# Optimization experiments

Hardware: AMD Instinct MI355X
Metric: run time of the kernel (lower is better)

The kernel has to match this reference:

```python
import jax, jax.numpy as jnp
import numpy as np

D_MODEL = 1024
D_STATE = 16
EXPAND = 2
D_CONV = 4
D_INNER = EXPAND * D_MODEL          # 2048
DT_RANK = D_MODEL // 16             # 64
B = 2
L = 1024
EPS = 1e-5


def setup_inputs() -> dict:
    key = jax.random.key(0)
    ks = jax.random.split(key, 8)
    s = 0.02
    return {
        "x": jax.random.normal(ks[0], (B, L, D_MODEL), jnp.float32),
        "ln_gamma": jnp.ones((D_MODEL,), jnp.float32),
        "ln_beta": jnp.zeros((D_MODEL,), jnp.float32),
        "in_proj_w": jax.random.normal(ks[1], (2 * D_INNER, D_MODEL), jnp.float32) * s,
        "conv_w": jax.random.normal(ks[2], (D_INNER, 1, D_CONV), jnp.float32) * s,
        "conv_b": jnp.zeros((D_INNER,), jnp.float32),
        "x_proj_w": jax.random.normal(ks[3], (DT_RANK + 2 * D_STATE, D_INNER), jnp.float32) * s,
        "dt_proj_w": jax.random.normal(ks[4], (D_INNER, DT_RANK), jnp.float32) * s,
        "dt_proj_b": jax.random.normal(ks[5], (D_INNER,), jnp.float32) * 0.01,
        "A_log": jnp.log(jnp.tile(jnp.arange(1, D_STATE + 1, dtype=jnp.float32), (D_INNER, 1))),
        "D_skip": jnp.ones((D_INNER,), jnp.float32),
        "out_proj_w": jax.random.normal(ks[6], (D_MODEL, D_INNER), jnp.float32) * s,
    }


def _layernorm(x, g, b):
    mu = jnp.mean(x, axis=-1, keepdims=True)
    var = jnp.mean((x - mu) ** 2, axis=-1, keepdims=True)
    return (x - mu) * jax.lax.rsqrt(var + EPS) * g + b


def _mamba_forward(x, ln_gamma, ln_beta, in_proj_w, conv_w, conv_b,
                   x_proj_w, dt_proj_w, dt_proj_b, A_log, D_skip, out_proj_w):
    residual = x
    xn = _layernorm(x, ln_gamma, ln_beta)

    # in_proj -> split into ssm input u and gate z   (b, l, 2*d_inner)
    xz = jnp.einsum('bld,ed->ble', xn, in_proj_w)
    u, z = jnp.split(xz, 2, axis=-1)

    # causal depthwise conv1d (padding = d_conv-1 on the left, truncated to L)
    uc = jnp.transpose(u, (0, 2, 1))  # (b, d_inner, l)
    uc = jax.lax.conv_general_dilated(
        uc, conv_w, window_strides=(1,), padding=[(D_CONV - 1, 0)],
        feature_group_count=D_INNER,
        dimension_numbers=('NCH', 'OIH', 'NCH'))
    uc = uc + conv_b[None, :, None]
    u = jax.nn.silu(jnp.transpose(uc, (0, 2, 1)))  # (b, l, d_inner)

    # selective SSM
    A = -jnp.exp(A_log)                              # (d_inner, d_state)
    x_dbl = jnp.einsum('bld,ed->ble', u, x_proj_w)   # (b, l, dt_rank+2*n)
    dt, Bm, Cm = jnp.split(x_dbl, [DT_RANK, DT_RANK + D_STATE], axis=-1)
    delta = jax.nn.softplus(jnp.einsum('blr,dr->bld', dt, dt_proj_w) + dt_proj_b)

    def step(h, inputs):
        d_t, B_t, C_t, u_t = inputs            # (b,di) (b,n) (b,n) (b,di)
        dA = jnp.exp(d_t[..., None] * A)       # (b, di, n)
        h = dA * h + (d_t * u_t)[..., None] * B_t[:, None, :]
        y = jnp.einsum('bdn,bn->bd', h, C_t)
        return h, y

    h0 = jnp.zeros((x.shape[0], D_INNER, D_STATE), x.dtype)
    xs = (jnp.moveaxis(delta, 1, 0), jnp.moveaxis(Bm, 1, 0),
          jnp.moveaxis(Cm, 1, 0), jnp.moveaxis(u, 1, 0))
    _, ys = jax.lax.scan(step, h0, xs)
    y = jnp.moveaxis(ys, 0, 1) + u * D_skip     # (b, l, d_inner)

    y = y * jax.nn.silu(z)                      # gated output
    out = jnp.einsum('ble,de->bld', y, out_proj_w)
    # dropout is identity in eval mode
    return out + residual


def reference(x, ln_gamma, ln_beta, in_proj_w, conv_w, conv_b,
              x_proj_w, dt_proj_w, dt_proj_b, A_log, D_skip, out_proj_w):
    return _mamba_forward(x, ln_gamma, ln_beta, in_proj_w, conv_w, conv_b,
                          x_proj_w, dt_proj_w, dt_proj_b, A_log, D_skip, out_proj_w)
```

## Files before the change

### kernel.cpp

```cpp
#include <hip/hip_runtime.h>

#define D_MODEL 1024
#define D_STATE 16
#define D_INNER 2048
#define DT_RANK 64
#define NBATCH 2
#define SEQ_L 1024
#define M_ROWS (NBATCH * SEQ_L)
#define CHUNK 32
#define NCHUNK (SEQ_L / CHUNK)

typedef __bf16 bf16x8 __attribute__((ext_vector_type(8)));
typedef float f32x4 __attribute__((ext_vector_type(4)));
typedef unsigned short u16;
typedef unsigned int u32;
typedef u16 u16x4 __attribute__((ext_vector_type(4)));
typedef u16 u16x8 __attribute__((ext_vector_type(8)));

__device__ __forceinline__ float bf2f(u16 h) {
    return __uint_as_float(((unsigned)h) << 16);
}
__device__ __forceinline__ u16 f2bf(float f) {
    unsigned u = __float_as_uint(f);
    u += 0x7fff + ((u >> 16) & 1);
    return (u16)(u >> 16);
}

__global__ __launch_bounds__(256) void prep(
    const float* __restrict__ s0, const float* __restrict__ s1,
    const float* __restrict__ s2, const float* __restrict__ s3,
    u16* __restrict__ d0, u16* __restrict__ d1,
    u16* __restrict__ d2, u16* __restrict__ d3,
    const float* __restrict__ x, const float* __restrict__ g,
    const float* __restrict__ b, u16* __restrict__ xn) {
    int blk = blockIdx.x;
    if (blk < 6464) {
        int idx = blk * 256 + threadIdx.x;
        const float4* s; u16* dp; int i;
        if (idx < 1048576)      { s = (const float4*)s0; i = idx;           dp = d0; }
        else if (idx < 1572864) { s = (const float4*)s1; i = idx - 1048576; dp = d1; }
        else if (idx < 1622016) { s = (const float4*)s2; i = idx - 1572864; dp = d2; }
        else                    { s = (const float4*)s3; i = idx - 1622016; dp = d3; }
        float4 v = s[i];
        u16x4 o = {f2bf(v.x), f2bf(v.y), f2bf(v.z), f2bf(v.w)};
        *(u16x4*)(dp + (size_t)i * 4) = o;
        return;
    }
    int row = blk - 6464;
    const float4* xr = (const float4*)(x + (size_t)row * D_MODEL);
    float4 v = xr[threadIdx.x];
    float s  = v.x + v.y + v.z + v.w;
    float ss = v.x * v.x + v.y * v.y + v.z * v.z + v.w * v.w;
#pragma unroll
    for (int off = 32; off > 0; off >>= 1) {
        s  += __shfl_down(s,  off, 64);
        ss += __shfl_down(ss, off, 64);
    }
    __shared__ float sh_s[4], sh_ss[4];
    int wid = threadIdx.x >> 6;
    if ((threadIdx.x & 63) == 0) { sh_s[wid] = s; sh_ss[wid] = ss; }
    __syncthreads();
    float mu  = (sh_s[0] + sh_s[1] + sh_s[2] + sh_s[3]) * (1.0f / D_MODEL);
    float var = (sh_ss[0] + sh_ss[1] + sh_ss[2] + sh_ss[3]) * (1.0f / D_MODEL) - mu * mu;
    float rs = rsqrtf(var + 1e-5f);
    int c0 = threadIdx.x * 4;
    float vv[4] = {v.x, v.y, v.z, v.w};
#pragma unroll
    for (int j = 0; j < 4; j++) {
        int c = c0 + j;
        float o = (vv[j] - mu) * rs * g[c] + b[c];
        xn[(size_t)row * D_MODEL + c] = f2bf(o);
    }
}

template <int BM, int BN, int WM, int WN, int MODE>
__global__ __launch_bounds__(256) void gemm_lds(
    const __bf16* __restrict__ A, const __bf16* __restrict__ W,
    int K, int Ksteps, int ldC,
    float* __restrict__ outF, u16* __restrict__ outB) {
    constexpr int WCOLS = BN / (WN * 16);
    __shared__ __bf16 As[BM * 32];
    __shared__ __bf16 Bs[BN * 32];
    int tid  = threadIdx.x;
    int lane = tid & 63;
    int wid  = tid >> 6;
    int l16  = lane & 15;
    int quad = lane >> 4;
    int wr = wid / WCOLS;
    int wc = wid % WCOLS;
    int m0 = blockIdx.y * BM;
    int n0 = blockIdx.x * BN;
    int kbase = blockIdx.z * Ksteps * 32;

    f32x4 acc[WM][WN];
#pragma unroll
    for (int mi = 0; mi < WM; mi++)
#pragma unroll
        for (int nj = 0; nj < WN; nj++)
            acc[mi][nj] = (f32x4){0.f, 0.f, 0.f, 0.f};

    for (int ki = 0; ki < Ksteps; ki++) {
        int k0 = kbase + ki * 32;
        __syncthreads();
#pragma unroll
        for (int i = 0; i < BM / 64; i++) {
            int t   = i * 256 + tid;
            int row = t >> 2;
            int cg  = (t & 3) ^ ((row >> 1) & 3);
            __builtin_amdgcn_global_load_lds(
                (const __attribute__((address_space(1))) u32*)(A + (size_t)(m0 + row) * K + k0 + cg * 8),
                (__attribute__((address_space(3))) u32*)(As + (i * 256 + wid * 64) * 8),
                16, 0, 0);
        }
#pragma unroll
        for (int i = 0; i < BN / 64; i++) {
            int t   = i * 256 + tid;
            int row = t >> 2;
            int cg  = (t & 3) ^ ((row >> 1) & 3);
            __builtin_amdgcn_global_load_lds(
                (const __attribute__((address_space(1))) u32*)(W + (size_t)(n0 + row) * K + k0 + cg * 8),
                (__attribute__((address_space(3))) u32*)(Bs + (i * 256 + wid * 64) * 8),
                16, 0, 0);
        }
        __syncthreads();

        bf16x8 af[WM], bfr[WN];
#pragma unroll
        for (int mi = 0; mi < WM; mi++) {
            int r  = wr * WM * 16 + mi * 16 + l16;
            int cg = quad ^ ((r >> 1) & 3);
            af[mi] = *(const bf16x8*)(As + r * 32 + cg * 8);
        }
#pragma unroll
        for (int nj = 0; nj < WN; nj++) {
            int r  = wc * WN * 16 + nj * 16 + l16;
            int cg = quad ^ ((r >> 1) & 3);
            bfr[nj] = *(const bf16x8*)(Bs + r * 32 + cg * 8);
        }
#pragma unroll
        for (int mi = 0; mi < WM; mi++)
#pragma unroll
            for (int nj = 0; nj < WN; nj++)
                acc[mi][nj] = __builtin_amdgcn_mfma_f32_16x16x32_bf16(
                    af[mi], bfr[nj], acc[mi][nj], 0, 0, 0);
    }

    float* outP = (MODE == 4) ? outF + (size_t)blockIdx.z * M_ROWS * ldC : outF;
#pragma unroll
    for (int mi = 0; mi < WM; mi++) {
#pragma unroll
        for (int nj = 0; nj < WN; nj++) {
            int col = n0 + wc * WN * 16 + nj * 16 + l16;
#pragma unroll
            for (int r = 0; r < 4; r++) {
                int row = m0 + wr * WM * 16 + mi * 16 + quad * 4 + r;
                float v = acc[mi][nj][r];
                if (MODE == 0) {
                    outB[(size_t)row * ldC + col] = f2bf(v);
                } else {
                    outP[(size_t)row * ldC + col] = v;
                }
            }
        }
    }
}

__global__ __launch_bounds__(256) void out_reduce(
    const float* __restrict__ p, const float* __restrict__ x,
    float* __restrict__ out) {
    int idx = blockIdx.x * 256 + threadIdx.x;
    const int N = M_ROWS * D_MODEL;
    float4 a = ((const float4*)p)[idx];
    float4 b = ((const float4*)(p + N))[idx];
    float4 c = ((const float4*)(p + 2 * N))[idx];
    float4 d = ((const float4*)(p + 3 * N))[idx];
    float4 r = ((const float4*)x)[idx];
    float4 o;
    o.x = a.x + b.x + c.x + d.x + r.x;
    o.y = a.y + b.y + c.y + d.y + r.y;
    o.z = a.z + b.z + c.z + d.z + r.z;
    o.w = a.w + b.w + c.w + d.w + r.w;
    ((float4*)out)[idx] = o;
}

template <int MODE>
__global__ __launch_bounds__(256) void gemm_bt(
    const __bf16* __restrict__ A, const __bf16* __restrict__ W,
    int K, int Ksplit, int Nw, int ldC,
    float* __restrict__ outF, u16* __restrict__ outB16,
    const float* __restrict__ auxF) {
    int lane = threadIdx.x & 63;
    int wid  = threadIdx.x >> 6;
    int m0 = blockIdx.y * 64;
    int n0 = blockIdx.x * 64;
    int kc = blockIdx.z;
    int l16  = lane & 15;
    int quad = lane >> 4;
    int mrow = m0 + wid * 16 + l16;

    const __bf16* ap = A + (size_t)mrow * K + kc * Ksplit + quad * 8;
    const __bf16* wp[4];
#pragma unroll
    for (int j = 0; j < 4; j++) {
        int nc = n0 + j * 16 + l16;
        if (nc > Nw - 1) nc = Nw - 1;
        wp[j] = W + (size_t)nc * K + kc * Ksplit + quad * 8;
    }
    f32x4 acc[4];
#pragma unroll
    for (int j = 0; j < 4; j++) acc[j] = (f32x4){0.f, 0.f, 0.f, 0.f};

    for (int k = 0; k < Ksplit; k += 32) {
        bf16x8 a = *(const bf16x8*)ap;
        ap += 32;
#pragma unroll
        for (int j = 0; j < 4; j++) {
            bf16x8 bfr = *(const bf16x8*)wp[j];
            wp[j] += 32;
            acc[j] = __builtin_amdgcn_mfma_f32_16x16x32_bf16(a, bfr, acc[j], 0, 0, 0);
        }
    }
    float* out = (MODE == 1) ? outF + (size_t)kc * (M_ROWS * 96) : outF;
#pragma unroll
    for (int j = 0; j < 4; j++) {
        int col = n0 + j * 16 + l16;
#pragma unroll
        for (int r = 0; r < 4; r++) {
            int row = m0 + wid * 16 + quad * 4 + r;
            float v = acc[j][r];
            if (MODE == 1) {
                if (col < Nw) out[(size_t)row * ldC + col] = v;
            } else {
                float t = v + auxF[col];
                float sp = (t > 20.f) ? t : log1pf(__expf(t));
                outB16[(size_t)row * ldC + col] = f2bf(sp);
            }
        }
    }
}

__global__ __launch_bounds__(256) void xdbl_reduce(
    const float* __restrict__ xdp, float* __restrict__ xd,
    u16* __restrict__ dtb) {
    int idx = blockIdx.x * 256 + threadIdx.x;
    const int N = M_ROWS * 96;
    float v = 0.f;
#pragma unroll
    for (int i = 0; i < 8; i++) v += xdp[idx + i * N];
    xd[idx] = v;
    int mrow = idx / 96;
    int r = idx - mrow * 96;
    if (r < DT_RANK) dtb[mrow * DT_RANK + r] = f2bf(v);
}

__global__ __launch_bounds__(256) void conv_silu(
    const u16* __restrict__ xz, const float* __restrict__ cw,
    const float* __restrict__ cb, u16* __restrict__ uc) {
    int idx = blockIdx.x * 256 + threadIdx.x;
    int base = idx * 8;
    int d = base & (D_INNER - 1);
    int m = base >> 11;
    int t = m & (SEQ_L - 1);
    float s[8];
    {
        float4 b0 = *(const float4*)(cb + d);
        float4 b1 = *(const float4*)(cb + d + 4);
        s[0] = b0.x; s[1] = b0.y; s[2] = b0.z; s[3] = b0.w;
        s[4] = b1.x; s[5] = b1.y; s[6] = b1.z; s[7] = b1.w;
    }
#pragma unroll
    for (int j = 0; j < 4; j++) {
        int tt = t - 3 + j;
        if (tt >= 0) {
            u16x8 uv = *(const u16x8*)(xz + (size_t)(m - 3 + j) * (2 * D_INNER) + d);
#pragma unroll
            for (int q = 0; q < 8; q++) {
                s[q] += cw[(d + q) * 4 + j] * bf2f(uv[q]);
            }
        }
    }
    u16x8 o;
#pragma unroll
    for (int q = 0; q < 8; q++) {
        float sig = 1.f / (1.f + __expf(-s[q]));
        o[q] = f2bf(s[q] * sig);
    }
    *(u16x8*)(uc + base) = o;
}

__global__ __launch_bounds__(256) void scan_chunk(
    const u16* __restrict__ delta, const u16* __restrict__ uc,
    const float* __restrict__ xd, const float* __restrict__ A_log,
    float* __restrict__ Pst, float* __restrict__ Sst) {
    __shared__ float Bsh[CHUNK][16];
    int tid  = threadIdx.x;
    int lane = tid & 63;
    int w    = tid >> 6;
    int dsub = lane & 15;
    int g    = lane >> 4;
    int n0   = g * 4;
    int c = blockIdx.x, b = blockIdx.z;
    int d = blockIdx.y * 64 + w * 16 + dsub;
    int mbase = b * SEQ_L + c * CHUNK;

    if (tid < CHUNK * 4) {
        int row = tid >> 2, q = tid & 3;
        *(float4*)&Bsh[row][q * 4] =
            *(const float4*)(xd + (size_t)(mbase + row) * 96 + DT_RANK + q * 4);
    }
    __syncthreads();

    float a[4];
    {
        float4 a0 = *(const float4*)(A_log + d * D_STATE + n0);
        a[0] = -__expf(a0.x); a[1] = -__expf(a0.y);
        a[2] = -__expf(a0.z); a[3] = -__expf(a0.w);
    }
    float P[4] = {1.f, 1.f, 1.f, 1.f}, S[4] = {0.f, 0.f, 0.f, 0.f};

    for (int t0 = 0; t0 < CHUNK; t0 += 4) {
        float dlv[4], uv[4];
#pragma unroll
        for (int i = 0; i < 4; i++) {
            int m = mbase + t0 + i;
            dlv[i] = bf2f(delta[(size_t)m * D_INNER + d]);
            uv[i]  = bf2f(uc[(size_t)m * D_INNER + d]);
        }
#pragma unroll
        for (int i = 0; i < 4; i++) {
            float c1 = dlv[i] * uv[i];
#pragma unroll
            for (int j = 0; j < 4; j++) {
                float dA = __expf(dlv[i] * a[j]);
                P[j] *= dA;
                S[j] = dA * S[j] + c1 * Bsh[t0 + i][n0 + j];
            }
        }
    }
    size_t s = ((size_t)(b * D_INNER + d) * NCHUNK + c) * D_STATE + n0;
    *(float4*)(Pst + s) = (float4){P[0], P[1], P[2], P[3]};
    *(float4*)(Sst + s) = (float4){S[0], S[1], S[2], S[3]};
}

__global__ __launch_bounds__(256) void scan_combine(
    const float* __restrict__ Pst, const float* __restrict__ Sst,
    float* __restrict__ Hin) {
    int idx = blockIdx.x * 256 + threadIdx.x;
    int bd = idx >> 4;
    int n  = idx & 15;
    float h = 0.f;
#pragma unroll
    for (int c = 0; c < NCHUNK; ++c) {
        size_t s = ((size_t)bd * NCHUNK + c) * D_STATE + n;
        Hin[s] = h;
        h = Pst[s] * h + Sst[s];
    }
}

__global__ __launch_bounds__(256) void scan_apply(
    const u16* __restrict__ delta, const u16* __restrict__ uc,
    const float* __restrict__ xd, const u16* __restrict__ xz,
    const float* __restrict__ A_log, const float* __restrict__ Dsk,
    const float* __restrict__ Hin, u16* __restrict__ yg) {
    __shared__ float BCs[CHUNK][32];
    int tid  = threadIdx.x;
    int lane = tid & 63;
    int w    = tid >> 6;
    int dsub = lane & 15;
    int g    = lane >> 4;
    int n0   = g * 4;
    int c = blockIdx.x, b = blockIdx.z;
    int d = blockIdx.y * 64 + w * 16 + dsub;
    int mbase = b * SEQ_L + c * CHUNK;

    {
        int row = tid >> 3, q = tid & 7;
        *(float4*)&BCs[row][q * 4] =
            *(const float4*)(xd + (size_t)(mbase + row) * 96 + DT_RANK + q * 4);
    }
    __syncthreads();

    float a[4];
    {
        float4 a0 = *(const float4*)(A_log + d * D_STATE + n0);
        a[0] = -__expf(a0.x); a[1] = -__expf(a0.y);
        a[2] = -__expf(a0.z); a[3] = -__expf(a0.w);
    }
    float h[4];
    {
        float4 h0 = *(const float4*)(Hin +
            (((size_t)(b * D_INNER + d) * NCHUNK + c) * D_STATE + n0));
        h[0] = h0.x; h[1] = h0.y; h[2] = h0.z; h[3] = h0.w;
    }
    float dsk = Dsk[d];

    for (int t0 = 0; t0 < CHUNK; t0 += 4) {
        float dlv[4], uv[4], zv[4];
#pragma unroll
        for (int i = 0; i < 4; i++) {
            int m = mbase + t0 + i;
            dlv[i] = bf2f(delta[(size_t)m * D_INNER + d]);
            uv[i]  = bf2f(uc[(size_t)m * D_INNER + d]);
            zv[i]  = bf2f(xz[(size_t)m * (2 * D_INNER) + D_INNER + d]);
        }
#pragma unroll
        for (int i = 0; i < 4; i++) {
            int t = t0 + i;
            float c1 = dlv[i] * uv[i];
            float y = 0.f;
#pragma unroll
            for (int j = 0; j < 4; j++) {
                float dA = __expf(dlv[i] * a[j]);
                h[j] = dA * h[j] + c1 * BCs[t][n0 + j];
                y += h[j] * BCs[t][16 + n0 + j];
            }
            y += __shfl_xor(y, 16);
            y += __shfl_xor(y, 32);
            if (g == 0) {
                float z = zv[i];
                float yv = y + uv[i] * dsk;
                float gt = z / (1.f + __expf(-z));
                yg[(size_t)(mbase + t) * D_INNER + d] = f2bf(yv * gt);
            }
        }
    }
}

extern "C" void kernel_launch(void* const* d_in, const int* in_sizes, int n_in,
                              void* d_out, int out_size, void* d_ws, size_t ws_size,
                              hipStream_t stream) {
    const float* x         = (const float*)d_in[0];
    const float* ln_g      = (const float*)d_in[1];
    const float* ln_b      = (const float*)d_in[2];
    const float* in_proj_w = (const float*)d_in[3];
    const float* conv_w    = (const float*)d_in[4];
    const float* conv_b    = (const float*)d_in[5];
    const float* x_proj_w  = (const float*)d_in[6];
    const float* dt_proj_w = (const float*)d_in[7];
    const float* dt_proj_b = (const float*)d_in[8];
    const float* A_log     = (const float*)d_in[9];
    const float* Dsk       = (const float*)d_in[10];
    const float* out_proj_w= (const float*)d_in[11];

    char* ws = (char*)d_ws;
    u16* xn   = (u16*)ws;    ws += (size_t)M_ROWS * D_MODEL * 2;
    u16* xz   = (u16*)ws;    ws += (size_t)M_ROWS * 2 * D_INNER * 2;
    u16* ucv  = (u16*)ws;    ws += (size_t)M_ROWS * D_INNER * 2;
    float* xd = (float*)ws;  ws += (size_t)M_ROWS * 96 * 4;
    u16* dtb  = (u16*)ws;    ws += (size_t)M_ROWS * DT_RANK * 2;
    u16* dl   = (u16*)ws;    ws += (size_t)M_ROWS * D_INNER * 2;
    u16* yg   = (u16*)ws;    ws += (size_t)M_ROWS * D_INNER * 2;
    u16* w_in = (u16*)ws;    ws += (size_t)4194304 * 2;
    u16* w_out= (u16*)ws;    ws += (size_t)2097152 * 2;
    u16* w_xp = (u16*)ws;    ws += (size_t)196608 * 2;
    u16* w_dt = (u16*)ws;    ws += (size_t)131072 * 2;
    float* Pst = (float*)ws; ws += (size_t)NBATCH * D_INNER * D_STATE * NCHUNK * 4;
    float* Sst = (float*)ws; ws += (size_t)NBATCH * D_INNER * D_STATE * NCHUNK * 4;
    float* Hin = (float*)ws; ws += (size_t)NBATCH * D_INNER * D_STATE * NCHUNK * 4;
    float* xdp = (float*)ws; ws += (size_t)8 * M_ROWS * 96 * 4;
    float* opart = (float*)ws;

    prep<<<6464 + M_ROWS, 256, 0, stream>>>(
        in_proj_w, out_proj_w, x_proj_w, dt_proj_w, w_in, w_out, w_xp, w_dt,
        x, ln_g, ln_b, xn);
    gemm_lds<128, 128, 4, 4, 0><<<dim3(4096 / 128, M_ROWS / 128, 1), 256, 0, stream>>>(
        (const __bf16*)xn, (const __bf16*)w_in, D_MODEL, D_MODEL / 32, 2 * D_INNER,
        nullptr, xz);
    conv_silu<<<(M_ROWS * D_INNER) / (256 * 8), 256, 0, stream>>>(xz, conv_w, conv_b, ucv);
    gemm_bt<1><<<dim3(2, 32, 8), 256, 0, stream>>>(
        (const __bf16*)ucv, (const __bf16*)w_xp, D_INNER, D_INNER / 8, 96, 96,
        xdp, nullptr, nullptr);
    xdbl_reduce<<<(M_ROWS * 96) / 256, 256, 0, stream>>>(xdp, xd, dtb);
    gemm_bt<2><<<dim3(32, 32, 1), 256, 0, stream>>>(
        (const __bf16*)dtb, (const __bf16*)w_dt, DT_RANK, DT_RANK, D_INNER,
        D_INNER, nullptr, dl, dt_proj_b);
    dim3 sgrid(NCHUNK, D_INNER / 64, NBATCH);
    scan_chunk<<<sgrid, 256, 0, stream>>>(dl, ucv, xd, A_log, Pst, Sst);
    scan_combine<<<(NBATCH * D_INNER * D_STATE) / 256, 256, 0, stream>>>(Pst, Sst, Hin);
    scan_apply<<<sgrid, 256, 0, stream>>>(dl, ucv, xd, xz, A_log, Dsk, Hin, yg);
    gemm_lds<128, 128, 4, 4, 4><<<dim3(1024 / 128, M_ROWS / 128, 4), 256, 0, stream>>>(
        (const __bf16*)yg, (const __bf16*)w_out, D_INNER, D_INNER / 4 / 32, D_MODEL,
        opart, nullptr);
    out_reduce<<<(M_ROWS * D_MODEL / 4) / 256, 256, 0, stream>>>(
        opart, x, (float*)d_out);
}
```

Before: 275.5 us.

## Replace chunked three-pass scan with single sequential fused scan kernel

Drops the chunk/combine/apply scan decomposition and adds one kernel in which each block walks the full sequence for 16 channels. One lane holds each state element, the C-dot reduction uses DPP adds, and the next chunk's delta/u/z/B/C inputs are double-buffered through LDS. This removes two kernel launches, the P/S/Hin round trips through global memory, and the duplicated recurrence work. The cost is that only 256 blocks each run a serial 1024-step loop, which may expose latency. Both large GEMMs also move from 128x128 to 64x128 tiles to raise block count.

```diff
diff --git a/kernel.cpp b/kernel.cpp
--- a/kernel.cpp
+++ b/kernel.cpp
@@ -16,6 +16,7 @@
 typedef unsigned int u32;
 typedef u16 u16x4 __attribute__((ext_vector_type(4)));
 typedef u16 u16x8 __attribute__((ext_vector_type(8)));
+typedef u32 u32x4 __attribute__((ext_vector_type(4)));
 
 __device__ __forceinline__ float bf2f(u16 h) {
     return __uint_as_float(((unsigned)h) << 16);
@@ -288,140 +289,98 @@
     *(u16x8*)(uc + base) = o;
 }
 
-__global__ __launch_bounds__(256) void scan_chunk(
-    const u16* __restrict__ delta, const u16* __restrict__ uc,
-    const float* __restrict__ xd, const float* __restrict__ A_log,
-    float* __restrict__ Pst, float* __restrict__ Sst) {
-    __shared__ float Bsh[CHUNK][16];
-    int tid  = threadIdx.x;
-    int lane = tid & 63;
-    int w    = tid >> 6;
-    int dsub = lane & 15;
-    int g    = lane >> 4;
-    int n0   = g * 4;
-    int c = blockIdx.x, b = blockIdx.z;
-    int d = blockIdx.y * 64 + w * 16 + dsub;
-    int mbase = b * SEQ_L + c * CHUNK;
-
-    if (tid < CHUNK * 4) {
-        int row = tid >> 2, q = tid & 3;
-        *(float4*)&Bsh[row][q * 4] =
-            *(const float4*)(xd + (size_t)(mbase + row) * 96 + DT_RANK + q * 4);
-    }
-    __syncthreads();
-
-    float a[4];
-    {
-        float4 a0 = *(const float4*)(A_log + d * D_STATE + n0);
-        a[0] = -__expf(a0.x); a[1] = -__expf(a0.y);
-        a[2] = -__expf(a0.z); a[3] = -__expf(a0.w);
-    }
-    float P[4] = {1.f, 1.f, 1.f, 1.f}, S[4] = {0.f, 0.f, 0.f, 0.f};
-
-    for (int t0 = 0; t0 < CHUNK; t0 += 4) {
-        float dlv[4], uv[4];
-#pragma unroll
-        for (int i = 0; i < 4; i++) {
-            int m = mbase + t0 + i;
-            dlv[i] = bf2f(delta[(size_t)m * D_INNER + d]);
-            uv[i]  = bf2f(uc[(size_t)m * D_INNER + d]);
-        }
-#pragma unroll
-        for (int i = 0; i < 4; i++) {
-            float c1 = dlv[i] * uv[i];
-#pragma unroll
-            for (int j = 0; j < 4; j++) {
-                float dA = __expf(dlv[i] * a[j]);
-                P[j] *= dA;
-                S[j] = dA * S[j] + c1 * Bsh[t0 + i][n0 + j];
-            }
-        }
-    }
-    size_t s = ((size_t)(b * D_INNER + d) * NCHUNK + c) * D_STATE + n0;
-    *(float4*)(Pst + s) = (float4){P[0], P[1], P[2], P[3]};
-    *(float4*)(Sst + s) = (float4){S[0], S[1], S[2], S[3]};
-}
-
-__global__ __launch_bounds__(256) void scan_combine(
-    const float* __restrict__ Pst, const float* __restrict__ Sst,
-    float* __restrict__ Hin) {
-    int idx = blockIdx.x * 256 + threadIdx.x;
-    int bd = idx >> 4;
-    int n  = idx & 15;
-    float h = 0.f;
-#pragma unroll
-    for (int c = 0; c < NCHUNK; ++c) {
-        size_t s = ((size_t)bd * NCHUNK + c) * D_STATE + n;
-        Hin[s] = h;
-        h = Pst[s] * h + Sst[s];
-    }
-}
-
-__global__ __launch_bounds__(256) void scan_apply(
-    const u16* __restrict__ delta, const u16* __restrict__ uc,
+template <int CTRL>
+__device__ __forceinline__ float dpp_add(float y) {
+    int s = __builtin_amdgcn_update_dpp(0, __float_as_int(y), CTRL, 0xf, 0xf, true);
+    return y + __int_as_float(s);
+}
+
+__global__ __launch_bounds__(256) void scan_fused(
+    const u16* __restrict__ delta, const u16* __restrict__ ucv,
     const float* __restrict__ xd, const u16* __restrict__ xz,
     const float* __restrict__ A_log, const float* __restrict__ Dsk,
-    const float* __restrict__ Hin, u16* __restrict__ yg) {
-    __shared__ float BCs[CHUNK][32];
-    int tid  = threadIdx.x;
-    int lane = tid & 63;
-    int w    = tid >> 6;
-    int dsub = lane & 15;
-    int g    = lane >> 4;
-    int n0   = g * 4;
-    int c = blockIdx.x, b = blockIdx.z;
-    int d = blockIdx.y * 64 + w * 16 + dsub;
-    int mbase = b * SEQ_L + c * CHUNK;
-
-    {
-        int row = tid >> 3, q = tid & 7;
-        *(float4*)&BCs[row][q * 4] =
-            *(const float4*)(xd + (size_t)(mbase + row) * 96 + DT_RANK + q * 4);
-    }
+    u16* __restrict__ yg) {
+    __shared__ u32  duz[2][CHUNK][16];
+    __shared__ u16  zb [2][CHUNK][16];
+    __shared__ float bc[2][CHUNK][32];
+
+    int tid = threadIdx.x;
+    int l   = tid & 63;
+    int w   = tid >> 6;
+    int dl_ = w * 4 + (l >> 4);
+    int n   = l & 15;
+    int b   = blockIdx.x >> 7;
+    int d0  = (blockIdx.x & 127) * 16;
+    int d   = d0 + dl_;
+
+    float a   = -__expf(A_log[d * D_STATE + n]);
+    float dsk = Dsk[d];
+    float h   = 0.f;
+
+    int srow  = (tid & 63) >> 1;
+    int shalf = tid & 1;
+    int bcrow = tid >> 3;
+    int bcq   = tid & 7;
+
+    u16x8 r_dl, r_uc, r_z; float4 r_bc;
+
+    auto issue = [&](int c) {
+        int mb = b * SEQ_L + c * CHUNK;
+        if (tid < 64) {
+            size_t off = (size_t)(mb + srow) * D_INNER + d0 + shalf * 8;
+            r_dl = *(const u16x8*)(delta + off);
+            r_uc = *(const u16x8*)(ucv + off);
+        } else if (tid < 128) {
+            r_z = *(const u16x8*)(xz + (size_t)(mb + srow) * (2 * D_INNER) + D_INNER + d0 + shalf * 8);
+        }
+        r_bc = *(const float4*)(xd + (size_t)(mb + bcrow) * 96 + DT_RANK + bcq * 4);
+    };
+    auto wr_lds = [&](int pb) {
+        if (tid < 64) {
+            u32 pk[8];
+#pragma unroll
+            for (int k = 0; k < 8; k++)
+                pk[k] = ((u32)r_dl[k] << 16) | (u32)r_uc[k];
+            *(u32x4*)&duz[pb][srow][shalf * 8]     = *(u32x4*)&pk[0];
+            *(u32x4*)&duz[pb][srow][shalf * 8 + 4] = *(u32x4*)&pk[4];
+        } else if (tid < 128) {
+            *(u16x8*)&zb[pb][srow][shalf * 8] = r_z;
+        }
+        *(float4*)&bc[pb][bcrow][bcq * 4] = r_bc;
+    };
+
+    issue(0);
+    wr_lds(0);
     __syncthreads();
 
-    float a[4];
-    {
-        float4 a0 = *(const float4*)(A_log + d * D_STATE + n0);
-        a[0] = -__expf(a0.x); a[1] = -__expf(a0.y);
-        a[2] = -__expf(a0.z); a[3] = -__expf(a0.w);
-    }
-    float h[4];
-    {
-        float4 h0 = *(const float4*)(Hin +
-            (((size_t)(b * D_INNER + d) * NCHUNK + c) * D_STATE + n0));
-        h[0] = h0.x; h[1] = h0.y; h[2] = h0.z; h[3] = h0.w;
-    }
-    float dsk = Dsk[d];
-
-    for (int t0 = 0; t0 < CHUNK; t0 += 4) {
-        float dlv[4], uv[4], zv[4];
-#pragma unroll
-        for (int i = 0; i < 4; i++) {
-            int m = mbase + t0 + i;
-            dlv[i] = bf2f(delta[(size_t)m * D_INNER + d]);
-            uv[i]  = bf2f(uc[(size_t)m * D_INNER + d]);
-            zv[i]  = bf2f(xz[(size_t)m * (2 * D_INNER) + D_INNER + d]);
-        }
-#pragma unroll
-        for (int i = 0; i < 4; i++) {
-            int t = t0 + i;
-            float c1 = dlv[i] * uv[i];
-            float y = 0.f;
-#pragma unroll
-            for (int j = 0; j < 4; j++) {
-                float dA = __expf(dlv[i] * a[j]);
-                h[j] = dA * h[j] + c1 * BCs[t][n0 + j];
-                y += h[j] * BCs[t][16 + n0 + j];
-            }
-            y += __shfl_xor(y, 16);
-            y += __shfl_xor(y, 32);
-            if (g == 0) {
-                float z = zv[i];
-                float yv = y + uv[i] * dsk;
-                float gt = z / (1.f + __expf(-z));
-                yg[(size_t)(mbase + t) * D_INNER + d] = f2bf(yv * gt);
-            }
+    for (int c = 0; c < NCHUNK; c++) {
+        int pb = c & 1;
+        if (c + 1 < NCHUNK) issue(c + 1);
+        int mb = b * SEQ_L + c * CHUNK;
+#pragma unroll 8
+        for (int t = 0; t < CHUNK; t++) {
+            u32 pv   = duz[pb][t][dl_];
+            float dlf = __uint_as_float(pv & 0xffff0000u);
+            float uf  = __uint_as_float(pv << 16);
+            float Bv  = bc[pb][t][n];
+            float Cv  = bc[pb][t][16 + n];
+            float dA  = __expf(dlf * a);
+            h = dA * h + (dlf * uf) * Bv;
+            float y = h * Cv;
+            y = dpp_add<0xB1>(y);
+            y = dpp_add<0x4E>(y);
+            y = dpp_add<0x124>(y);
+            y = dpp_add<0x128>(y);
+            float z  = bf2f(zb[pb][t][dl_]);
+            float gt = z / (1.f + __expf(-z));
+            float yv = (y + uf * dsk) * gt;
+            if (n == 0)
+                yg[(size_t)(mb + t) * D_INNER + d] = f2bf(yv);
+        }
+        __syncthreads();
+        if (c + 1 < NCHUNK) {
+            wr_lds((c + 1) & 1);
+            __syncthreads();
         }
     }
 }
@@ -454,16 +413,13 @@
     u16* w_out= (u16*)ws;    ws += (size_t)2097152 * 2;
     u16* w_xp = (u16*)ws;    ws += (size_t)196608 * 2;
     u16* w_dt = (u16*)ws;    ws += (size_t)131072 * 2;
-    float* Pst = (float*)ws; ws += (size_t)NBATCH * D_INNER * D_STATE * NCHUNK * 4;
-    float* Sst = (float*)ws; ws += (size_t)NBATCH * D_INNER * D_STATE * NCHUNK * 4;
-    float* Hin = (float*)ws; ws += (size_t)NBATCH * D_INNER * D_STATE * NCHUNK * 4;
     float* xdp = (float*)ws; ws += (size_t)8 * M_ROWS * 96 * 4;
     float* opart = (float*)ws;
 
     prep<<<6464 + M_ROWS, 256, 0, stream>>>(
         in_proj_w, out_proj_w, x_proj_w, dt_proj_w, w_in, w_out, w_xp, w_dt,
         x, ln_g, ln_b, xn);
-    gemm_lds<128, 128, 4, 4, 0><<<dim3(4096 / 128, M_ROWS / 128, 1), 256, 0, stream>>>(
+    gemm_lds<64, 128, 4, 2, 0><<<dim3(4096 / 128, M_ROWS / 64, 1), 256, 0, stream>>>(
         (const __bf16*)xn, (const __bf16*)w_in, D_MODEL, D_MODEL / 32, 2 * D_INNER,
         nullptr, xz);
     conv_silu<<<(M_ROWS * D_INNER) / (256 * 8), 256, 0, stream>>>(xz, conv_w, conv_b, ucv);
@@ -474,11 +430,8 @@
     gemm_bt<2><<<dim3(32, 32, 1), 256, 0, stream>>>(
         (const __bf16*)dtb, (const __bf16*)w_dt, DT_RANK, DT_RANK, D_INNER,
         D_INNER, nullptr, dl, dt_proj_b);
-    dim3 sgrid(NCHUNK, D_INNER / 64, NBATCH);
-    scan_chunk<<<sgrid, 256, 0, stream>>>(dl, ucv, xd, A_log, Pst, Sst);
-    scan_combine<<<(NBATCH * D_INNER * D_STATE) / 256, 256, 0, stream>>>(Pst, Sst, Hin);
-    scan_apply<<<sgrid, 256, 0, stream>>>(dl, ucv, xd, xz, A_log, Dsk, Hin, yg);
-    gemm_lds<128, 128, 4, 4, 4><<<dim3(1024 / 128, M_ROWS / 128, 4), 256, 0, stream>>>(
+    scan_fused<<<256, 256, 0, stream>>>(dl, ucv, xd, xz, A_log, Dsk, yg);
+    gemm_lds<64, 128, 4, 2, 4><<<dim3(1024 / 128, M_ROWS / 64, 4), 256, 0, stream>>>(
         (const __bf16*)yg, (const __bf16*)w_out, D_INNER, D_INNER / 4 / 32, D_MODEL,
         opart, nullptr);
     out_reduce<<<(M_ROWS * D_MODEL / 4) / 256, 256, 0, stream>>>(
```

Result: slower. 417.9 us (+51.7%).

## Replace x_proj split-K reduce kernel with atomics and fuse bf16 cast into dt_proj

Applied to the files above, without the earlier changes.

The split-K partials buffer and xdbl_reduce kernel are removed. gemm_xp now accumulates into xd with float atomicAdd, and prep gains extra blocks that zero xd first. gemm_dt reads fp32 xd directly and converts to bf16 in registers, so the dtb buffer is no longer needed. Separately, both gemm_lds launches switch to 64x128 tiles to put more blocks on the GPU. The aim is one fewer launch and less intermediate traffic, at the cost of atomic contention and summation order that is no longer deterministic.

```diff
diff --git a/kernel.cpp b/kernel.cpp
--- a/kernel.cpp
+++ b/kernel.cpp
@@ -32,7 +32,8 @@
     u16* __restrict__ d0, u16* __restrict__ d1,
     u16* __restrict__ d2, u16* __restrict__ d3,
     const float* __restrict__ x, const float* __restrict__ g,
-    const float* __restrict__ b, u16* __restrict__ xn) {
+    const float* __restrict__ b, u16* __restrict__ xn,
+    float* __restrict__ xd) {
     int blk = blockIdx.x;
     if (blk < 6464) {
         int idx = blk * 256 + threadIdx.x;
@@ -46,7 +47,12 @@
         *(u16x4*)(dp + (size_t)i * 4) = o;
         return;
     }
-    int row = blk - 6464;
+    if (blk < 6656) {
+        int zi = (blk - 6464) * 256 + threadIdx.x;
+        ((float4*)xd)[zi] = (float4){0.f, 0.f, 0.f, 0.f};
+        return;
+    }
+    int row = blk - 6656;
     const float4* xr = (const float4*)(x + (size_t)row * D_MODEL);
     float4 v = xr[threadIdx.x];
     float s  = v.x + v.y + v.z + v.w;
@@ -183,12 +189,10 @@
     ((float4*)out)[idx] = o;
 }
 
-template <int MODE>
-__global__ __launch_bounds__(256) void gemm_bt(
+__global__ __launch_bounds__(256) void gemm_xp(
     const __bf16* __restrict__ A, const __bf16* __restrict__ W,
-    int K, int Ksplit, int Nw, int ldC,
-    float* __restrict__ outF, u16* __restrict__ outB16,
-    const float* __restrict__ auxF) {
+    float* __restrict__ outF) {
+    const int K = D_INNER, Ksplit = D_INNER / 8, Nw = 96;
     int lane = threadIdx.x & 63;
     int wid  = threadIdx.x >> 6;
     int m0 = blockIdx.y * 64;
@@ -220,37 +224,68 @@
             acc[j] = __builtin_amdgcn_mfma_f32_16x16x32_bf16(a, bfr, acc[j], 0, 0, 0);
         }
     }
-    float* out = (MODE == 1) ? outF + (size_t)kc * (M_ROWS * 96) : outF;
 #pragma unroll
     for (int j = 0; j < 4; j++) {
         int col = n0 + j * 16 + l16;
+        if (col < Nw) {
+#pragma unroll
+            for (int r = 0; r < 4; r++) {
+                int row = m0 + wid * 16 + quad * 4 + r;
+                atomicAdd(outF + (size_t)row * 96 + col, acc[j][r]);
+            }
+        }
+    }
+}
+
+__global__ __launch_bounds__(256) void gemm_dt(
+    const float* __restrict__ A, const __bf16* __restrict__ W,
+    const float* __restrict__ bias, u16* __restrict__ outB16) {
+    int lane = threadIdx.x & 63;
+    int wid  = threadIdx.x >> 6;
+    int m0 = blockIdx.y * 64;
+    int n0 = blockIdx.x * 64;
+    int l16  = lane & 15;
+    int quad = lane >> 4;
+    int mrow = m0 + wid * 16 + l16;
+
+    const float* ap = A + (size_t)mrow * 96 + quad * 8;
+    const __bf16* wp[4];
+#pragma unroll
+    for (int j = 0; j < 4; j++) {
+        int nc = n0 + j * 16 + l16;
+        wp[j] = W + (size_t)nc * DT_RANK + quad * 8;
+    }
+    f32x4 acc[4];
+#pragma unroll
+    for (int j = 0; j < 4; j++) acc[j] = (f32x4){0.f, 0.f, 0.f, 0.f};
+
+#pragma unroll
+    for (int k = 0; k < DT_RANK; k += 32) {
+        float4 v0 = *(const float4*)(ap);
+        float4 v1 = *(const float4*)(ap + 4);
+        ap += 32;
+        u16x8 pk;
+        pk[0] = f2bf(v0.x); pk[1] = f2bf(v0.y); pk[2] = f2bf(v0.z); pk[3] = f2bf(v0.w);
+        pk[4] = f2bf(v1.x); pk[5] = f2bf(v1.y); pk[6] = f2bf(v1.z); pk[7] = f2bf(v1.w);
+        bf16x8 a = __builtin_bit_cast(bf16x8, pk);
+#pragma unroll
+        for (int j = 0; j < 4; j++) {
+            bf16x8 bfr = *(const bf16x8*)wp[j];
+            wp[j] += 32;
+            acc[j] = __builtin_amdgcn_mfma_f32_16x16x32_bf16(a, bfr, acc[j], 0, 0, 0);
+        }
+    }
+#pragma unroll
+    for (int j = 0; j < 4; j++) {
+        int col = n0 + j * 16 + l16;
 #pragma unroll
         for (int r = 0; r < 4; r++) {
             int row = m0 + wid * 16 + quad * 4 + r;
-            float v = acc[j][r];
-            if (MODE == 1) {
-                if (col < Nw) out[(size_t)row * ldC + col] = v;
-            } else {
-                float t = v + auxF[col];
-                float sp = (t > 20.f) ? t : log1pf(__expf(t));
-                outB16[(size_t)row * ldC + col] = f2bf(sp);
-            }
-        }
-    }
-}
-
-__global__ __launch_bounds__(256) void xdbl_reduce(
-    const float* __restrict__ xdp, float* __restrict__ xd,
-    u16* __restrict__ dtb) {
-    int idx = blockIdx.x * 256 + threadIdx.x;
-    const int N = M_ROWS * 96;
-    float v = 0.f;
-#pragma unroll
-    for (int i = 0; i < 8; i++) v += xdp[idx + i * N];
-    xd[idx] = v;
-    int mrow = idx / 96;
-    int r = idx - mrow * 96;
-    if (r < DT_RANK) dtb[mrow * DT_RANK + r] = f2bf(v);
+            float t = acc[j][r] + bias[col];
+            float sp = (t > 20.f) ? t : log1pf(__expf(t));
+            outB16[(size_t)row * D_INNER + col] = f2bf(sp);
+        }
+    }
 }
 
 __global__ __launch_bounds__(256) void conv_silu(
@@ -447,7 +482,6 @@
     u16* xz   = (u16*)ws;    ws += (size_t)M_ROWS * 2 * D_INNER * 2;
     u16* ucv  = (u16*)ws;    ws += (size_t)M_ROWS * D_INNER * 2;
     float* xd = (float*)ws;  ws += (size_t)M_ROWS * 96 * 4;
-    u16* dtb  = (u16*)ws;    ws += (size_t)M_ROWS * DT_RANK * 2;
     u16* dl   = (u16*)ws;    ws += (size_t)M_ROWS * D_INNER * 2;
     u16* yg   = (u16*)ws;    ws += (size_t)M_ROWS * D_INNER * 2;
     u16* w_in = (u16*)ws;    ws += (size_t)4194304 * 2;
@@ -457,28 +491,24 @@
     float* Pst = (float*)ws; ws += (size_t)NBATCH * D_INNER * D_STATE * NCHUNK * 4;
     float* Sst = (float*)ws; ws += (size_t)NBATCH * D_INNER * D_STATE * NCHUNK * 4;
     float* Hin = (float*)ws; ws += (size_t)NBATCH * D_INNER * D_STATE * NCHUNK * 4;
-    float* xdp = (float*)ws; ws += (size_t)8 * M_ROWS * 96 * 4;
     float* opart = (float*)ws;
 
-    prep<<<6464 + M_ROWS, 256, 0, stream>>>(
+    prep<<<6656 + M_ROWS, 256, 0, stream>>>(
         in_proj_w, out_proj_w, x_proj_w, dt_proj_w, w_in, w_out, w_xp, w_dt,
-        x, ln_g, ln_b, xn);
-    gemm_lds<128, 128, 4, 4, 0><<<dim3(4096 / 128, M_ROWS / 128, 1), 256, 0, stream>>>(
+        x, ln_g, ln_b, xn, xd);
+    gemm_lds<64, 128, 4, 2, 0><<<dim3(4096 / 128, M_ROWS / 64, 1), 256, 0, stream>>>(
         (const __bf16*)xn, (const __bf16*)w_in, D_MODEL, D_MODEL / 32, 2 * D_INNER,
         nullptr, xz);
     conv_silu<<<(M_ROWS * D_INNER) / (256 * 8), 256, 0, stream>>>(xz, conv_w, conv_b, ucv);
-    gemm_bt<1><<<dim3(2, 32, 8), 256, 0, stream>>>(
-        (const __bf16*)ucv, (const __bf16*)w_xp, D_INNER, D_INNER / 8, 96, 96,
-        xdp, nullptr, nullptr);
-    xdbl_reduce<<<(M_ROWS * 96) / 256, 256, 0, stream>>>(xdp, xd, dtb);
-    gemm_bt<2><<<dim3(32, 32, 1), 256, 0, stream>>>(
-        (const __bf16*)dtb, (const __bf16*)w_dt, DT_RANK, DT_RANK, D_INNER,
-        D_INNER, nullptr, dl, dt_proj_b);
+    gemm_xp<<<dim3(2, 32, 8), 256, 0, stream>>>(
+        (const __bf16*)ucv, (const __bf16*)w_xp, xd);
+    gemm_dt<<<dim3(32, 32, 1), 256, 0, stream>>>(
+        xd, (const __bf16*)w_dt, dt_proj_b, dl);
     dim3 sgrid(NCHUNK, D_INNER / 64, NBATCH);
     scan_chunk<<<sgrid, 256, 0, stream>>>(dl, ucv, xd, A_log, Pst, Sst);
     scan_combine<<<(NBATCH * D_INNER * D_STATE) / 256, 256, 0, stream>>>(Pst, Sst, Hin);
     scan_apply<<<sgrid, 256, 0, stream>>>(dl, ucv, xd, xz, A_log, Dsk, Hin, yg);
-    gemm_lds<128, 128, 4, 4, 4><<<dim3(1024 / 128, M_ROWS / 128, 4), 256, 0, stream>>>(
+    gemm_lds<64, 128, 4, 2, 4><<<dim3(1024 / 128, M_ROWS / 64, 4), 256, 0, stream>>>(
         (const __bf16*)yg, (const __bf16*)w_out, D_INNER, D_INNER / 4 / 32, D_MODEL,
         opart, nullptr);
     out_reduce<<<(M_ROWS * D_MODEL / 4) / 256, 256, 0, stream>>>(
```

New measurement: 273.3 us. No clear change (-0.8%).
